# Kernel tuning notes

Measured on AMD Instinct MI355X. Metric: run time of the kernel, lower is better.

## Reference

```python
import jax, jax.numpy as jnp
import numpy as np

B, D, U, M, K = 8192, 512, 512, 16, 64


def setup_inputs() -> dict:
    key = jax.random.key(0)
    ks = jax.random.split(key, 5)
    return {
        "x": jax.random.normal(ks[0], (B, D), dtype=jnp.float32),
        "key_kernel": jax.random.normal(ks[1], (D, K), dtype=jnp.float32) * (1.0 / np.sqrt(D)),
        "key_bias": jnp.zeros((K,), dtype=jnp.float32),
        "keys_map": jax.random.normal(ks[2], (M, K), dtype=jnp.float32),
        "kernels": jax.random.normal(ks[3], (M, D, U), dtype=jnp.float32) * (1.0 / np.sqrt(D)),
        "biases": jnp.zeros((M, U), dtype=jnp.float32),
    }


def reference(x, key_kernel, key_bias, keys_map, kernels, biases):
    # key projection: [B, K]
    keyv = x @ key_kernel + key_bias
    # inverse-distance similarity to mode keys: [B, M]
    dist = jnp.sqrt(jnp.sum((keyv[:, None, :] - keys_map[None, :, :]) ** 2, axis=-1))
    sim = 1.0 / (dist + 1.0)
    modes = kernels.shape[0]
    # kernel = mean_m(sim_m * kernels_m); out = x @ kernel.
    # Distributive identity: out = (1/M) * sum_m sim_m * (x @ kernels_m)
    out = jnp.einsum("bm,bd,mdu->bu", sim, x, kernels) / modes
    # bias = mean_m(sim_m * biases_m): [B, U]
    out = out + (sim @ biases) / modes
    return out
```

## Files before the change

### kernel.cpp

```cpp
#include <hip/hip_runtime.h>
#include <hip/hip_bf16.h>
#include <stdint.h>

#define B_SZ 8192
#define D_SZ 512
#define U_SZ 512
#define M_SZ 16
#define K_SZ 64

typedef short bf16x8 __attribute__((ext_vector_type(8)));
typedef float f32x4 __attribute__((ext_vector_type(4)));

__device__ __forceinline__ unsigned short f2bf(float f) {
  union { float f; unsigned u; } v; v.f = f;
  unsigned r = v.u + 0x7fffu + ((v.u >> 16) & 1u);
  return (unsigned short)(r >> 16);
}

__global__ __launch_bounds__(256) void prep1(
    const float* __restrict__ x, const float* __restrict__ key_kernel,
    const float* __restrict__ kernels, unsigned short* __restrict__ xbf,
    unsigned short* __restrict__ kbf, unsigned short* __restrict__ wkbf) {
  __shared__ float tf[32][65];
  __shared__ unsigned short sx[16][520];
  int bid = blockIdx.x;
  int t = threadIdx.x;

  if (bid < 2048) {
    int m = bid >> 7;
    int rem = bid & 127;
    int a = (rem >> 3) & 15;
    int ut = rem & 7;
    int d0 = a * 32, u0 = ut * 64;
    {
      int dr = t >> 4, uc = t & 15;
      const float* src = kernels + ((size_t)m * D_SZ + d0 + dr) * U_SZ + u0 + uc * 4;
      float4 aa = *(const float4*)src;
      float4 bb = *(const float4*)(src + (size_t)16 * U_SZ);
      tf[dr][uc * 4 + 0] = aa.x; tf[dr][uc * 4 + 1] = aa.y;
      tf[dr][uc * 4 + 2] = aa.z; tf[dr][uc * 4 + 3] = aa.w;
      tf[dr + 16][uc * 4 + 0] = bb.x; tf[dr + 16][uc * 4 + 1] = bb.y;
      tf[dr + 16][uc * 4 + 2] = bb.z; tf[dr + 16][uc * 4 + 3] = bb.w;
    }
    __syncthreads();
    {
      int ur = t >> 2, dc = t & 3;
      int j = ur >> 4, lane16 = ur & 15;
      int kt = a >> 1, h = a & 1;
      unsigned short* dst = kbf +
          (((((size_t)m * 8 + ut) * 8 + kt) * 4 + j) * 2 + h) * 512 +
          ((size_t)dc * 16 + lane16) * 8;
      ushort4 lo, hi;
      lo.x = f2bf(tf[dc * 8 + 0][ur]); lo.y = f2bf(tf[dc * 8 + 1][ur]);
      lo.z = f2bf(tf[dc * 8 + 2][ur]); lo.w = f2bf(tf[dc * 8 + 3][ur]);
      hi.x = f2bf(tf[dc * 8 + 4][ur]); hi.y = f2bf(tf[dc * 8 + 5][ur]);
      hi.z = f2bf(tf[dc * 8 + 6][ur]); hi.w = f2bf(tf[dc * 8 + 7][ur]);
      *(ushort4*)dst = lo;
      *(ushort4*)(dst + 4) = hi;
    }
    return;
  }

  if (bid < 2056) {
    int kt = bid - 2048;
#pragma unroll
    for (int rep = 0; rep < 2; ++rep) {
      int c = rep * 256 + t;
      int j = c >> 7, h = (c >> 6) & 1, quad = (c >> 4) & 3, ln = c & 15;
      int dd = kt * 64 + h * 32 + quad * 8;
      int u = j * 16 + ln;
      unsigned short v[8];
#pragma unroll
      for (int e = 0; e < 8; ++e)
        v[e] = f2bf(key_kernel[(size_t)(dd + e) * K_SZ + u]);
      unsigned short* dst =
          wkbf + ((size_t)((kt * 4 + j) * 2 + h) * 64 + quad * 16 + ln) * 8;
#pragma unroll
      for (int e = 0; e < 8; ++e) dst[e] = v[e];
    }
    return;
  }

  {
    int xb0 = bid - 2056;
    int btx = xb0 >> 3, i = xb0 & 7;
    int b0 = xb0 * 16;
#pragma unroll
    for (int rep = 0; rep < 8; ++rep) {
      int idx = rep * 256 + t;
      int row = idx >> 7;
      int c4 = (idx & 127) * 4;
      float4 v = *(const float4*)(x + (size_t)(b0 + row) * D_SZ + c4);
      ushort4 o;
      o.x = f2bf(v.x); o.y = f2bf(v.y); o.z = f2bf(v.z); o.w = f2bf(v.w);
      *(ushort4*)(&sx[row][c4]) = o;
    }
    __syncthreads();
    int w = t >> 6, l = t & 63;
    int ln = l & 15, quad = l >> 4;
#pragma unroll
    for (int rep = 0; rep < 4; ++rep) {
      int c = w * 4 + rep;
      int kt = c >> 1, h = c & 1;
      const unsigned short* srcp = &sx[ln][kt * 64 + h * 32 + quad * 8];
      ushort4 lo = *(const ushort4*)(srcp);
      ushort4 hi = *(const ushort4*)(srcp + 4);
      unsigned short* dst =
          xbf + ((((size_t)btx * 8 + kt) * 8 + i) * 2 + h) * 512 + (size_t)l * 8;
      *(ushort4*)dst = lo;
      *(ushort4*)(dst + 4) = hi;
    }
  }
}

__global__ __launch_bounds__(256) void prep2(
    const unsigned short* __restrict__ xbf, const unsigned short* __restrict__ wkbf,
    const float* __restrict__ key_bias, const float* __restrict__ keys_map,
    float* __restrict__ simT) {
  __shared__ float kv[64][68];
  __shared__ float sKM[16][64];
  int t = threadIdx.x, w = t >> 6, l = t & 63;
  int blk = blockIdx.x;
  int b0 = blk * 64, bt = blk >> 1, ibase = (blk & 1) * 4;
  int lane16 = l & 15, quad = l >> 4;

  ((float4*)sKM)[t] = ((const float4*)keys_map)[t];

  f32x4 acc[4];
#pragma unroll
  for (int j = 0; j < 4; ++j) acc[j] = (f32x4){0.f, 0.f, 0.f, 0.f};

  for (int kt = 0; kt < 8; ++kt) {
    bf16x8 af[2];
#pragma unroll
    for (int h = 0; h < 2; ++h)
      af[h] = *(const bf16x8*)(xbf +
                               ((((size_t)bt * 8 + kt) * 8 + ibase + w) * 2 + h) * 512 +
                               (size_t)l * 8);
#pragma unroll
    for (int j = 0; j < 4; ++j) {
      bf16x8 b0f = *(const bf16x8*)(wkbf + ((size_t)((kt * 4 + j) * 2 + 0) * 64 + l) * 8);
      bf16x8 b1f = *(const bf16x8*)(wkbf + ((size_t)((kt * 4 + j) * 2 + 1) * 64 + l) * 8);
      acc[j] = __builtin_amdgcn_mfma_f32_16x16x32_bf16(af[0], b0f, acc[j], 0, 0, 0);
      acc[j] = __builtin_amdgcn_mfma_f32_16x16x32_bf16(af[1], b1f, acc[j], 0, 0, 0);
    }
  }
#pragma unroll
  for (int j = 0; j < 4; ++j) {
    float bc = key_bias[j * 16 + lane16];
#pragma unroll
    for (int r = 0; r < 4; ++r)
      kv[w * 16 + quad * 4 + r][j * 16 + lane16] = acc[j][r] + bc;
  }
  __syncthreads();

  int row = t >> 2, mg = (t & 3) * 4;
  float d2[4] = {0.f, 0.f, 0.f, 0.f};
#pragma unroll 8
  for (int k = 0; k < 64; ++k) {
    float kvv = kv[row][k];
#pragma unroll
    for (int q = 0; q < 4; ++q) {
      float df = kvv - sKM[mg + q][k];
      d2[q] += df * df;
    }
  }
#pragma unroll
  for (int q = 0; q < 4; ++q)
    simT[(size_t)(mg + q) * B_SZ + b0 + row] = 1.0f / (sqrtf(d2[q]) + 1.0f);
}

#define STAGE(mode_, kt_, bufi_)                                               \
  {                                                                            \
    const unsigned short* _src = kbf_l +                                       \
        (((size_t)(mode_) * 8 + ut) * 8 + (kt_)) * 4096 + w * 512;             \
    unsigned short* _dst = Bbuf + (bufi_) * 4096 + w * 512;                    \
    __builtin_amdgcn_global_load_lds(                                          \
        (const __attribute__((address_space(1))) unsigned int*)(_src),         \
        (__attribute__((address_space(3))) unsigned int*)(_dst), 16, 0, 0);    \
  }

#define LOAD_AF(dst_, kt_)                                                     \
  _Pragma("unroll") for (int ii = 0; ii < 2; ++ii)                             \
      _Pragma("unroll") for (int h = 0; h < 2; ++h) {                          \
    int g_ = bt * 16 + w * 2 + ii;                                             \
    dst_[ii][h] = *(const bf16x8*)(                                            \
        xbf + ((((size_t)(g_ >> 3) * 8 + (kt_)) * 8 + (g_ & 7)) * 2 + h) *     \
                  512 +                                                        \
              (size_t)l * 8);                                                  \
  }

__global__ __launch_bounds__(512, 2) void poly_gemm(
    const unsigned short* __restrict__ xbf,
    const unsigned short* __restrict__ kbf,
    const float* __restrict__ simT,
    const float* __restrict__ biases,
    float* __restrict__ out) {
  __shared__ __align__(16) char smem[86016];

  int t = threadIdx.x, w = t >> 6, l = t & 63;
  int bid = blockIdx.x;
  int ut = bid & 7, bt = bid >> 3;
  int b0 = bt * 256, u0 = ut * 64;
  int lane16 = l & 15, quad = l >> 4;

  unsigned short* Bbuf = (unsigned short*)smem;
  float* sSim = (float*)(smem + 65536);
  float* sBias = (float*)(smem + 81920);

  {
    int m = t >> 5, c = (t & 31) * 8;
    const float* src = simT + (size_t)m * B_SZ + b0 + c;
    float4* dst = (float4*)(sSim + m * 256 + c);
    dst[0] = ((const float4*)src)[0];
    dst[1] = ((const float4*)src)[1];
    int bi = t * 2;
    *(float2*)(sBias + bi) =
        *(const float2*)(biases + (size_t)(bi >> 6) * U_SZ + u0 + (bi & 63));
  }

  const unsigned short* kbf_l = kbf + (size_t)l * 8;

  bf16x8 afc[2][2], afn[2][2];

  STAGE(0, 0, 0);
  STAGE(1, 0, 1);
  STAGE(2, 0, 2);
  STAGE(3, 0, 3);
  LOAD_AF(afc, 0);
  asm volatile("s_waitcnt vmcnt(0)" ::: "memory");
  __syncthreads();

  f32x4 facc[2][4];
#pragma unroll
  for (int i = 0; i < 2; ++i)
#pragma unroll
    for (int j = 0; j < 4; ++j) facc[i][j] = (f32x4){0.f, 0.f, 0.f, 0.f};

#pragma unroll 1
  for (int kt = 0; kt < 8; ++kt) {
#pragma unroll
    for (int mode = 0; mode < 16; ++mode) {
      const int s = kt * 16 + mode;
      {
        int mode4 = (mode + 4) & 15;
        int kt4 = (mode >= 12) ? ((kt + 1) & 7) : kt;
        STAGE(mode4, kt4, (s + 4) & 7);
      }
      if (mode == 0 && kt < 7) { LOAD_AF(afn, kt + 1); }
      if (mode < 5) {
        if (kt < 7)
          asm volatile("s_waitcnt vmcnt(8)" ::: "memory");
        else
          asm volatile("s_waitcnt vmcnt(4)" ::: "memory");
      } else {
        asm volatile("s_waitcnt vmcnt(4)" ::: "memory");
      }
      asm volatile("s_barrier" ::: "memory");

      const unsigned short* lb = Bbuf + (s & 7) * 4096;
      bf16x8 bfr[4][2];
#pragma unroll
      for (int j = 0; j < 4; ++j)
#pragma unroll
        for (int h = 0; h < 2; ++h)
          bfr[j][h] = *(const bf16x8*)(lb + (j * 2 + h) * 512 + (size_t)l * 8);

      f32x4 sv[2];
#pragma unroll
      for (int i = 0; i < 2; ++i)
        sv[i] =
            *(const f32x4*)(sSim + mode * 256 + w * 32 + i * 16 + quad * 4);

#pragma unroll
      for (int i = 0; i < 2; ++i)
#pragma unroll
        for (int j = 0; j < 4; ++j) {
          f32x4 p = __builtin_amdgcn_mfma_f32_16x16x32_bf16(
              afc[i][0], bfr[j][0], (f32x4){0.f, 0.f, 0.f, 0.f}, 0, 0, 0);
          p = __builtin_amdgcn_mfma_f32_16x16x32_bf16(afc[i][1], bfr[j][1], p,
                                                      0, 0, 0);
#pragma unroll
          for (int r = 0; r < 4; ++r) facc[i][j][r] += sv[i][r] * p[r];
        }

      if (kt == 0) {
        float bbv[4];
#pragma unroll
        for (int j = 0; j < 4; ++j)
          bbv[j] = sBias[mode * 64 + j * 16 + lane16];
#pragma unroll
        for (int i = 0; i < 2; ++i)
#pragma unroll
          for (int j = 0; j < 4; ++j)
#pragma unroll
            for (int r = 0; r < 4; ++r) facc[i][j][r] += sv[i][r] * bbv[j];
      }
    }
    if (kt < 7) {
#pragma unroll
      for (int ii = 0; ii < 2; ++ii)
#pragma unroll
        for (int h = 0; h < 2; ++h) afc[ii][h] = afn[ii][h];
    }
  }

  asm volatile("s_waitcnt vmcnt(0)" ::: "memory");
#pragma unroll
  for (int i = 0; i < 2; ++i)
#pragma unroll
    for (int r = 0; r < 4; ++r) {
      int row = b0 + w * 32 + i * 16 + quad * 4 + r;
      float* orow = out + (size_t)row * U_SZ + u0;
#pragma unroll
      for (int j = 0; j < 4; ++j)
        orow[j * 16 + lane16] = facc[i][j][r] * 0.0625f;
    }
}

extern "C" void kernel_launch(void* const* d_in, const int* in_sizes, int n_in,
                              void* d_out, int out_size, void* d_ws, size_t ws_size,
                              hipStream_t stream) {
  const float* x = (const float*)d_in[0];
  const float* key_kernel = (const float*)d_in[1];
  const float* key_bias = (const float*)d_in[2];
  const float* keys_map = (const float*)d_in[3];
  const float* kernels = (const float*)d_in[4];
  const float* biases = (const float*)d_in[5];
  float* out = (float*)d_out;

  char* p = (char*)d_ws;
  unsigned short* xbf = (unsigned short*)p;  p += (size_t)B_SZ * D_SZ * 2;
  unsigned short* kbf = (unsigned short*)p;  p += (size_t)M_SZ * U_SZ * D_SZ * 2;
  unsigned short* wkbf = (unsigned short*)p; p += (size_t)K_SZ * D_SZ * 2;
  float* simT = (float*)p;

  prep1<<<dim3(2568), 256, 0, stream>>>(x, key_kernel, kernels, xbf, kbf, wkbf);
  prep2<<<dim3(128), 256, 0, stream>>>(xbf, wkbf, key_bias, keys_map, simT);
  poly_gemm<<<dim3(256), 512, 0, stream>>>(xbf, kbf, simT, biases, out);
}
```

Before: 163.4 us.

## Split modes across wave pairs with 64-row tiles and LDS cross-wave reduction

Each wave now handles 64 rows (four 16-row MFMA tiles) and half of the 16 modes instead of 32 rows and all modes. Each LDS B tile is therefore reused across more A rows per wave, and the number of barriered steps per k-tile drops from 16 to 8. The two mode halves are summed through LDS before the store. The prep kernel's kbf write pattern is also changed to a contiguous per-lane layout. The costs are doubled accumulator and A-fragment registers, which may hurt occupancy under the 2-blocks launch bound, and an extra LDS reduction at the end.

```diff
diff --git a/kernel.cpp b/kernel.cpp
--- a/kernel.cpp
+++ b/kernel.cpp
@@ -44,12 +44,14 @@
     }
     __syncthreads();
     {
-      int ur = t >> 2, dc = t & 3;
-      int j = ur >> 4, lane16 = ur & 15;
+      int j = t >> 6;
+      int lp = t & 63;
+      int dc = lp >> 4, lane16 = lp & 15;
       int kt = a >> 1, h = a & 1;
+      int ur = j * 16 + lane16;
       unsigned short* dst = kbf +
           (((((size_t)m * 8 + ut) * 8 + kt) * 4 + j) * 2 + h) * 512 +
-          ((size_t)dc * 16 + lane16) * 8;
+          (size_t)lp * 8;
       ushort4 lo, hi;
       lo.x = f2bf(tf[dc * 8 + 0][ur]); lo.y = f2bf(tf[dc * 8 + 1][ur]);
       lo.z = f2bf(tf[dc * 8 + 2][ur]); lo.w = f2bf(tf[dc * 8 + 3][ur]);
@@ -170,20 +172,26 @@
     simT[(size_t)(mg + q) * B_SZ + b0 + row] = 1.0f / (sqrtf(d2[q]) + 1.0f);
 }
 
-#define STAGE(mode_, kt_, bufi_)                                               \
+#define GLL(src_, dst_)                                                        \
+  __builtin_amdgcn_global_load_lds(                                            \
+      (const __attribute__((address_space(1))) unsigned int*)(src_),           \
+      (__attribute__((address_space(3))) unsigned int*)(dst_), 16, 0, 0)
+
+#define STAGE(mi_, kt_, slot_)                                                 \
   {                                                                            \
     const unsigned short* _src = kbf_l +                                       \
-        (((size_t)(mode_) * 8 + ut) * 8 + (kt_)) * 4096 + w * 512;             \
-    unsigned short* _dst = Bbuf + (bufi_) * 4096 + w * 512;                    \
-    __builtin_amdgcn_global_load_lds(                                          \
-        (const __attribute__((address_space(1))) unsigned int*)(_src),         \
-        (__attribute__((address_space(3))) unsigned int*)(_dst), 16, 0, 0);    \
+        (((size_t)((w & 1) * 8 + (mi_)) * 8 + ut) * 8 + (kt_)) * 4096 +        \
+        (w >> 1) * 1024;                                                       \
+    unsigned short* _dst =                                                     \
+        Bbuf + ((slot_) * 2 + (w & 1)) * 4096 + (w >> 1) * 1024;               \
+    GLL(_src, _dst);                                                           \
+    GLL(_src + 512, _dst + 512);                                               \
   }
 
 #define LOAD_AF(dst_, kt_)                                                     \
-  _Pragma("unroll") for (int ii = 0; ii < 2; ++ii)                             \
+  _Pragma("unroll") for (int ii = 0; ii < 4; ++ii)                             \
       _Pragma("unroll") for (int h = 0; h < 2; ++h) {                          \
-    int g_ = bt * 16 + w * 2 + ii;                                             \
+    int g_ = bt * 16 + rg * 4 + ii;                                            \
     dst_[ii][h] = *(const bf16x8*)(                                            \
         xbf + ((((size_t)(g_ >> 3) * 8 + (kt_)) * 8 + (g_ & 7)) * 2 + h) *     \
                   512 +                                                        \
@@ -202,6 +210,7 @@
   int bid = blockIdx.x;
   int ut = bid & 7, bt = bid >> 3;
   int b0 = bt * 256, u0 = ut * 64;
+  int rg = w >> 1, half = w & 1;
   int lane16 = l & 15, quad = l >> 4;
 
   unsigned short* Bbuf = (unsigned short*)smem;
@@ -221,44 +230,39 @@
 
   const unsigned short* kbf_l = kbf + (size_t)l * 8;
 
-  bf16x8 afc[2][2], afn[2][2];
+  bf16x8 afc[4][2], afn[4][2];
 
   STAGE(0, 0, 0);
   STAGE(1, 0, 1);
-  STAGE(2, 0, 2);
-  STAGE(3, 0, 3);
   LOAD_AF(afc, 0);
   asm volatile("s_waitcnt vmcnt(0)" ::: "memory");
   __syncthreads();
 
-  f32x4 facc[2][4];
-#pragma unroll
-  for (int i = 0; i < 2; ++i)
+  f32x4 facc[4][4];
+#pragma unroll
+  for (int i = 0; i < 4; ++i)
 #pragma unroll
     for (int j = 0; j < 4; ++j) facc[i][j] = (f32x4){0.f, 0.f, 0.f, 0.f};
 
 #pragma unroll 1
   for (int kt = 0; kt < 8; ++kt) {
 #pragma unroll
-    for (int mode = 0; mode < 16; ++mode) {
-      const int s = kt * 16 + mode;
+    for (int mi = 0; mi < 8; ++mi) {
+      const int s = kt * 8 + mi;
+      const int mode = half * 8 + mi;
       {
-        int mode4 = (mode + 4) & 15;
-        int kt4 = (mode >= 12) ? ((kt + 1) & 7) : kt;
-        STAGE(mode4, kt4, (s + 4) & 7);
+        int mi2 = (mi + 2) & 7;
+        int kt2 = (mi >= 6) ? ((kt + 1) & 7) : kt;
+        STAGE(mi2, kt2, (s + 2) & 3);
       }
-      if (mode == 0 && kt < 7) { LOAD_AF(afn, kt + 1); }
-      if (mode < 5) {
-        if (kt < 7)
-          asm volatile("s_waitcnt vmcnt(8)" ::: "memory");
-        else
-          asm volatile("s_waitcnt vmcnt(4)" ::: "memory");
-      } else {
+      if (mi == 0 && kt < 7) { LOAD_AF(afn, kt + 1); }
+      if (mi < 3 && kt < 7)
+        asm volatile("s_waitcnt vmcnt(12)" ::: "memory");
+      else
         asm volatile("s_waitcnt vmcnt(4)" ::: "memory");
-      }
       asm volatile("s_barrier" ::: "memory");
 
-      const unsigned short* lb = Bbuf + (s & 7) * 4096;
+      const unsigned short* lb = Bbuf + ((s & 3) * 2 + half) * 4096;
       bf16x8 bfr[4][2];
 #pragma unroll
       for (int j = 0; j < 4; ++j)
@@ -266,14 +270,14 @@
         for (int h = 0; h < 2; ++h)
           bfr[j][h] = *(const bf16x8*)(lb + (j * 2 + h) * 512 + (size_t)l * 8);
 
-      f32x4 sv[2];
-#pragma unroll
-      for (int i = 0; i < 2; ++i)
-        sv[i] =
-            *(const f32x4*)(sSim + mode * 256 + w * 32 + i * 16 + quad * 4);
-
-#pragma unroll
-      for (int i = 0; i < 2; ++i)
+      f32x4 sv[4];
+#pragma unroll
+      for (int i = 0; i < 4; ++i)
+        sv[i] = *(const f32x4*)(sSim + mode * 256 + rg * 64 + i * 16 +
+                                quad * 4);
+
+#pragma unroll
+      for (int i = 0; i < 4; ++i)
 #pragma unroll
         for (int j = 0; j < 4; ++j) {
           f32x4 p = __builtin_amdgcn_mfma_f32_16x16x32_bf16(
@@ -290,7 +294,7 @@
         for (int j = 0; j < 4; ++j)
           bbv[j] = sBias[mode * 64 + j * 16 + lane16];
 #pragma unroll
-        for (int i = 0; i < 2; ++i)
+        for (int i = 0; i < 4; ++i)
 #pragma unroll
           for (int j = 0; j < 4; ++j)
 #pragma unroll
@@ -299,23 +303,41 @@
     }
     if (kt < 7) {
 #pragma unroll
-      for (int ii = 0; ii < 2; ++ii)
+      for (int ii = 0; ii < 4; ++ii)
 #pragma unroll
         for (int h = 0; h < 2; ++h) afc[ii][h] = afn[ii][h];
     }
   }
 
   asm volatile("s_waitcnt vmcnt(0)" ::: "memory");
-#pragma unroll
-  for (int i = 0; i < 2; ++i)
-#pragma unroll
-    for (int r = 0; r < 4; ++r) {
-      int row = b0 + w * 32 + i * 16 + quad * 4 + r;
-      float* orow = out + (size_t)row * U_SZ + u0;
-#pragma unroll
-      for (int j = 0; j < 4; ++j)
-        orow[j * 16 + lane16] = facc[i][j][r] * 0.0625f;
-    }
+  __syncthreads();
+  float* sRed = (float*)smem;
+  if (half == 1) {
+#pragma unroll
+    for (int i = 0; i < 4; ++i)
+#pragma unroll
+      for (int r = 0; r < 4; ++r)
+#pragma unroll
+        for (int j = 0; j < 4; ++j)
+          sRed[(rg * 64 + i * 16 + quad * 4 + r) * 68 + j * 16 + lane16] =
+              facc[i][j][r];
+  }
+  __syncthreads();
+  if (half == 0) {
+#pragma unroll
+    for (int i = 0; i < 4; ++i)
+#pragma unroll
+      for (int r = 0; r < 4; ++r) {
+        int row = b0 + rg * 64 + i * 16 + quad * 4 + r;
+        float* orow = out + (size_t)row * U_SZ + u0;
+#pragma unroll
+        for (int j = 0; j < 4; ++j)
+          orow[j * 16 + lane16] =
+              (facc[i][j][r] +
+               sRed[(rg * 64 + i * 16 + quad * 4 + r) * 68 + j * 16 + lane16]) *
+              0.0625f;
+      }
+  }
 }
 
 extern "C" void kernel_launch(void* const* d_in, const int* in_sizes, int n_in,
```

New measurement: 173.3 us. 6.1% more time.

## Fuse key projection and similarity into main GEMM kernel, dropping prep2

Applied to the files above, without the earlier changes.

Removes the separate prep2 launch. Each poly_gemm block now computes the key projection for its 256 rows with MFMA, then the inverse-distance similarities, all in shared memory. This drops a kernel launch and the simT round trip through global memory. The cost is that the key projection is recomputed by all 8 u-tile blocks that share a batch tile, and shared memory per block grows, which may affect occupancy at 2 blocks per CU. It also reorders the thread-to-output mapping of the kbf transpose writes in prep1 so consecutive threads write contiguous 16-byte chunks.

```diff
diff --git a/kernel.cpp b/kernel.cpp
--- a/kernel.cpp
+++ b/kernel.cpp
@@ -44,12 +44,14 @@
     }
     __syncthreads();
     {
-      int ur = t >> 2, dc = t & 3;
-      int j = ur >> 4, lane16 = ur & 15;
+      int j = t >> 6;
+      int lp = t & 63;
+      int dc = lp >> 4, lane16 = lp & 15;
       int kt = a >> 1, h = a & 1;
+      int ur = j * 16 + lane16;
       unsigned short* dst = kbf +
           (((((size_t)m * 8 + ut) * 8 + kt) * 4 + j) * 2 + h) * 512 +
-          ((size_t)dc * 16 + lane16) * 8;
+          (size_t)lp * 8;
       ushort4 lo, hi;
       lo.x = f2bf(tf[dc * 8 + 0][ur]); lo.y = f2bf(tf[dc * 8 + 1][ur]);
       lo.z = f2bf(tf[dc * 8 + 2][ur]); lo.w = f2bf(tf[dc * 8 + 3][ur]);
@@ -113,71 +115,17 @@
   }
 }
 
-__global__ __launch_bounds__(256) void prep2(
-    const unsigned short* __restrict__ xbf, const unsigned short* __restrict__ wkbf,
-    const float* __restrict__ key_bias, const float* __restrict__ keys_map,
-    float* __restrict__ simT) {
-  __shared__ float kv[64][68];
-  __shared__ float sKM[16][64];
-  int t = threadIdx.x, w = t >> 6, l = t & 63;
-  int blk = blockIdx.x;
-  int b0 = blk * 64, bt = blk >> 1, ibase = (blk & 1) * 4;
-  int lane16 = l & 15, quad = l >> 4;
-
-  ((float4*)sKM)[t] = ((const float4*)keys_map)[t];
-
-  f32x4 acc[4];
-#pragma unroll
-  for (int j = 0; j < 4; ++j) acc[j] = (f32x4){0.f, 0.f, 0.f, 0.f};
-
-  for (int kt = 0; kt < 8; ++kt) {
-    bf16x8 af[2];
-#pragma unroll
-    for (int h = 0; h < 2; ++h)
-      af[h] = *(const bf16x8*)(xbf +
-                               ((((size_t)bt * 8 + kt) * 8 + ibase + w) * 2 + h) * 512 +
-                               (size_t)l * 8);
-#pragma unroll
-    for (int j = 0; j < 4; ++j) {
-      bf16x8 b0f = *(const bf16x8*)(wkbf + ((size_t)((kt * 4 + j) * 2 + 0) * 64 + l) * 8);
-      bf16x8 b1f = *(const bf16x8*)(wkbf + ((size_t)((kt * 4 + j) * 2 + 1) * 64 + l) * 8);
-      acc[j] = __builtin_amdgcn_mfma_f32_16x16x32_bf16(af[0], b0f, acc[j], 0, 0, 0);
-      acc[j] = __builtin_amdgcn_mfma_f32_16x16x32_bf16(af[1], b1f, acc[j], 0, 0, 0);
-    }
-  }
-#pragma unroll
-  for (int j = 0; j < 4; ++j) {
-    float bc = key_bias[j * 16 + lane16];
-#pragma unroll
-    for (int r = 0; r < 4; ++r)
-      kv[w * 16 + quad * 4 + r][j * 16 + lane16] = acc[j][r] + bc;
-  }
-  __syncthreads();
-
-  int row = t >> 2, mg = (t & 3) * 4;
-  float d2[4] = {0.f, 0.f, 0.f, 0.f};
-#pragma unroll 8
-  for (int k = 0; k < 64; ++k) {
-    float kvv = kv[row][k];
-#pragma unroll
-    for (int q = 0; q < 4; ++q) {
-      float df = kvv - sKM[mg + q][k];
-      d2[q] += df * df;
-    }
-  }
-#pragma unroll
-  for (int q = 0; q < 4; ++q)
-    simT[(size_t)(mg + q) * B_SZ + b0 + row] = 1.0f / (sqrtf(d2[q]) + 1.0f);
-}
+#define GLL(src_, dst_)                                                        \
+  __builtin_amdgcn_global_load_lds(                                            \
+      (const __attribute__((address_space(1))) unsigned int*)(src_),           \
+      (__attribute__((address_space(3))) unsigned int*)(dst_), 16, 0, 0)
 
 #define STAGE(mode_, kt_, bufi_)                                               \
   {                                                                            \
     const unsigned short* _src = kbf_l +                                       \
         (((size_t)(mode_) * 8 + ut) * 8 + (kt_)) * 4096 + w * 512;             \
     unsigned short* _dst = Bbuf + (bufi_) * 4096 + w * 512;                    \
-    __builtin_amdgcn_global_load_lds(                                          \
-        (const __attribute__((address_space(1))) unsigned int*)(_src),         \
-        (__attribute__((address_space(3))) unsigned int*)(_dst), 16, 0, 0);    \
+    GLL(_src, _dst);                                                           \
   }
 
 #define LOAD_AF(dst_, kt_)                                                     \
@@ -193,10 +141,12 @@
 __global__ __launch_bounds__(512, 2) void poly_gemm(
     const unsigned short* __restrict__ xbf,
     const unsigned short* __restrict__ kbf,
-    const float* __restrict__ simT,
+    const unsigned short* __restrict__ wkbf,
+    const float* __restrict__ key_bias,
+    const float* __restrict__ keys_map,
     const float* __restrict__ biases,
     float* __restrict__ out) {
-  __shared__ __align__(16) char smem[86016];
+  __shared__ __align__(16) char smem[94208];
 
   int t = threadIdx.x, w = t >> 6, l = t & 63;
   int bid = blockIdx.x;
@@ -205,24 +155,71 @@
   int lane16 = l & 15, quad = l >> 4;
 
   unsigned short* Bbuf = (unsigned short*)smem;
-  float* sSim = (float*)(smem + 65536);
-  float* sBias = (float*)(smem + 81920);
+  float* kvp = (float*)smem;
+  float* sSim = (float*)(smem + 69632);
+  float* sBias = (float*)(smem + 86016);
+  float* sKM = (float*)(smem + 90112);
 
   {
-    int m = t >> 5, c = (t & 31) * 8;
-    const float* src = simT + (size_t)m * B_SZ + b0 + c;
-    float4* dst = (float4*)(sSim + m * 256 + c);
-    dst[0] = ((const float4*)src)[0];
-    dst[1] = ((const float4*)src)[1];
     int bi = t * 2;
     *(float2*)(sBias + bi) =
         *(const float2*)(biases + (size_t)(bi >> 6) * U_SZ + u0 + (bi & 63));
-  }
+    if (t < 256) ((float4*)sKM)[t] = ((const float4*)keys_map)[t];
+  }
+
+  {
+    f32x4 kacc[2][4];
+#pragma unroll
+    for (int ii = 0; ii < 2; ++ii)
+#pragma unroll
+      for (int j = 0; j < 4; ++j) kacc[ii][j] = (f32x4){0.f, 0.f, 0.f, 0.f};
+    for (int kt = 0; kt < 8; ++kt) {
+      bf16x8 a2[2][2];
+      LOAD_AF(a2, kt);
+#pragma unroll
+      for (int j = 0; j < 4; ++j) {
+        bf16x8 w0 = *(const bf16x8*)(wkbf + ((size_t)((kt * 4 + j) * 2 + 0) * 64 + l) * 8);
+        bf16x8 w1 = *(const bf16x8*)(wkbf + ((size_t)((kt * 4 + j) * 2 + 1) * 64 + l) * 8);
+#pragma unroll
+        for (int ii = 0; ii < 2; ++ii) {
+          kacc[ii][j] = __builtin_amdgcn_mfma_f32_16x16x32_bf16(a2[ii][0], w0, kacc[ii][j], 0, 0, 0);
+          kacc[ii][j] = __builtin_amdgcn_mfma_f32_16x16x32_bf16(a2[ii][1], w1, kacc[ii][j], 0, 0, 0);
+        }
+      }
+    }
+#pragma unroll
+    for (int j = 0; j < 4; ++j) {
+      float bc = key_bias[j * 16 + lane16];
+#pragma unroll
+      for (int ii = 0; ii < 2; ++ii)
+#pragma unroll
+        for (int r = 0; r < 4; ++r)
+          kvp[(size_t)(w * 32 + ii * 16 + quad * 4 + r) * 68 + j * 16 + lane16] =
+              kacc[ii][j][r] + bc;
+    }
+  }
+  __syncthreads();
+
+  {
+    int row = t >> 1, mg = (t & 1) * 8;
+    float d2[8] = {0.f, 0.f, 0.f, 0.f, 0.f, 0.f, 0.f, 0.f};
+#pragma unroll 8
+    for (int k = 0; k < 64; ++k) {
+      float kvv = kvp[(size_t)row * 68 + k];
+#pragma unroll
+      for (int q = 0; q < 8; ++q) {
+        float df = kvv - sKM[(mg + q) * 64 + k];
+        d2[q] += df * df;
+      }
+    }
+#pragma unroll
+    for (int q = 0; q < 8; ++q)
+      sSim[(mg + q) * 256 + row] = 1.0f / (sqrtf(d2[q]) + 1.0f);
+  }
+  __syncthreads();
 
   const unsigned short* kbf_l = kbf + (size_t)l * 8;
-
   bf16x8 afc[2][2], afn[2][2];
-
   STAGE(0, 0, 0);
   STAGE(1, 0, 1);
   STAGE(2, 0, 2);
@@ -332,10 +329,9 @@
   char* p = (char*)d_ws;
   unsigned short* xbf = (unsigned short*)p;  p += (size_t)B_SZ * D_SZ * 2;
   unsigned short* kbf = (unsigned short*)p;  p += (size_t)M_SZ * U_SZ * D_SZ * 2;
-  unsigned short* wkbf = (unsigned short*)p; p += (size_t)K_SZ * D_SZ * 2;
-  float* simT = (float*)p;
+  unsigned short* wkbf = (unsigned short*)p;
 
   prep1<<<dim3(2568), 256, 0, stream>>>(x, key_kernel, kernels, xbf, kbf, wkbf);
-  prep2<<<dim3(128), 256, 0, stream>>>(xbf, wkbf, key_bias, keys_map, simT);
-  poly_gemm<<<dim3(256), 512, 0, stream>>>(xbf, kbf, simT, biases, out);
+  poly_gemm<<<dim3(256), 512, 0, stream>>>(xbf, kbf, wkbf, key_bias, keys_map,
+                                           biases, out);
 }
```

Result: slower. 170.6 us (+4.4%).
